# Kernel optimization log

Hardware: AMD Instinct MI355X
Metric: run time of the kernel (lower is better)

Reference implementation:

```python
import jax, jax.numpy as jnp
import numpy as np

N, E, IN_DIM, HID = 50000, 800000, 512, 256
EPS = 1e-5


def _gat_layer(x, W, a_src, a_dst, b, src, dst, n, heads, ch):
    # x: [N, F_in] -> h: [N, H, C]
    h = (x @ W).reshape(n, heads, ch)
    alpha_src = jnp.sum(h * a_src, axis=-1)  # [N, H]
    alpha_dst = jnp.sum(h * a_dst, axis=-1)  # [N, H]
    e = jax.nn.leaky_relu(alpha_src[src] + alpha_dst[dst], negative_slope=0.2)  # [E', H]
    # segment softmax over incoming edges of each destination node
    m = jax.ops.segment_max(e, dst, num_segments=n)  # [N, H]
    ex = jnp.exp(e - m[dst])
    den = jax.ops.segment_sum(ex, dst, num_segments=n)  # [N, H]
    alpha = ex / den[dst]
    out = jax.ops.segment_sum(alpha[:, :, None] * h[src], dst, num_segments=n)  # [N, H, C]
    return out.reshape(n, heads * ch) + b


def _layer_norm(x, w, b):
    mu = jnp.mean(x, axis=-1, keepdims=True)
    var = jnp.mean(jnp.square(x - mu), axis=-1, keepdims=True)
    return (x - mu) * jax.lax.rsqrt(var + EPS) * w + b


def setup_inputs() -> dict:
    key = jax.random.key(0)
    ks = jax.random.split(key, 16)
    d = {}
    d['x'] = jax.random.normal(ks[0], (N, IN_DIM), dtype=jnp.float32)
    d['edge_index'] = jax.random.randint(ks[1], (2, E), 0, N, dtype=jnp.int32)
    s = 0.05
    # layer 0: GATConv(512, 64, heads=4)
    d['W0'] = jax.random.normal(ks[2], (IN_DIM, HID), dtype=jnp.float32) * s
    d['as0'] = jax.random.normal(ks[3], (4, 64), dtype=jnp.float32) * s
    d['ad0'] = jax.random.normal(ks[4], (4, 64), dtype=jnp.float32) * s
    d['b0'] = jnp.zeros((HID,), dtype=jnp.float32)
    d['lnw0'] = jnp.ones((HID,), dtype=jnp.float32)
    d['lnb0'] = jnp.zeros((HID,), dtype=jnp.float32)
    # layer 1: GATConv(256, 64, heads=4)
    d['W1'] = jax.random.normal(ks[5], (HID, HID), dtype=jnp.float32) * s
    d['as1'] = jax.random.normal(ks[6], (4, 64), dtype=jnp.float32) * s
    d['ad1'] = jax.random.normal(ks[7], (4, 64), dtype=jnp.float32) * s
    d['b1'] = jnp.zeros((HID,), dtype=jnp.float32)
    d['lnw1'] = jnp.ones((HID,), dtype=jnp.float32)
    d['lnb1'] = jnp.zeros((HID,), dtype=jnp.float32)
    # layer 2: GATConv(256, 256, heads=1)
    d['W2'] = jax.random.normal(ks[8], (HID, HID), dtype=jnp.float32) * s
    d['as2'] = jax.random.normal(ks[9], (1, HID), dtype=jnp.float32) * s
    d['ad2'] = jax.random.normal(ks[10], (1, HID), dtype=jnp.float32) * s
    d['b2'] = jnp.zeros((HID,), dtype=jnp.float32)
    d['lnw2'] = jnp.ones((HID,), dtype=jnp.float32)
    d['lnb2'] = jnp.zeros((HID,), dtype=jnp.float32)
    return d


def reference(x, edge_index, W0, as0, ad0, b0, lnw0, lnb0,
              W1, as1, ad1, b1, lnw1, lnb1,
              W2, as2, ad2, b2, lnw2, lnb2):
    n = x.shape[0]
    loop = jnp.arange(n, dtype=edge_index.dtype)
    src = jnp.concatenate([edge_index[0], loop])  # PyG add_self_loops=True
    dst = jnp.concatenate([edge_index[1], loop])
    h = _gat_layer(x, W0, as0, ad0, b0, src, dst, n, 4, 64)
    h = jax.nn.elu(_layer_norm(h, lnw0, lnb0))
    h = _gat_layer(h, W1, as1, ad1, b1, src, dst, n, 4, 64)
    h = jax.nn.elu(_layer_norm(h, lnw1, lnb1))
    h = _gat_layer(h, W2, as2, ad2, b2, src, dst, n, 1, HID)
    h = jax.nn.elu(_layer_norm(h, lnw2, lnb2))
    return h
```

## Files before the change

kernel.cpp:

```cpp
#include <hip/hip_runtime.h>

#define HID 256
#define EPSV 1e-5f
#define ASTR 136
#define BSTR 72

typedef __bf16 bf16x8 __attribute__((ext_vector_type(8)));
typedef float  floatx4 __attribute__((ext_vector_type(4)));

static __device__ __forceinline__ ushort f2bf(float f) {
  union { float f; unsigned int i; } c; c.f = f;
  unsigned int u = c.i;
  u += 0x7FFFu + ((u >> 16) & 1u);
  return (ushort)(u >> 16);
}
static __device__ __forceinline__ float bf2f(ushort u) {
  union { unsigned int i; float f; } c; c.i = ((unsigned int)u) << 16; return c.f;
}

__global__ void count_kernel(const int* __restrict__ ei, int* __restrict__ deg, int E, int tot) {
  int i = blockIdx.x * blockDim.x + threadIdx.x;
  if (i < tot) {
    int dst = (i < E) ? ei[E + i] : (i - E);
    atomicAdd(&deg[dst], 1);
  }
}

__global__ void scanA_kernel(const int* __restrict__ deg, int* __restrict__ incl,
                             int* __restrict__ sums, int n) {
  __shared__ int buf[1024];
  const int t = threadIdx.x;
  const int i = blockIdx.x * 1024 + t;
  int x = (i < n) ? deg[i] : 0;
  buf[t] = x;
  __syncthreads();
  for (int off = 1; off < 1024; off <<= 1) {
    int v = (t >= off) ? buf[t - off] : 0;
    __syncthreads();
    buf[t] += v;
    __syncthreads();
  }
  if (i < n) incl[i] = buf[t];
  if (t == 1023) sums[blockIdx.x] = buf[1023];
}

__global__ void scanB_kernel(int* __restrict__ sums, int* __restrict__ offs, int nblk) {
  __shared__ int buf[256];
  const int t = threadIdx.x;
  int x = (t < nblk) ? sums[t] : 0;
  buf[t] = x;
  __syncthreads();
  for (int off = 1; off < 256; off <<= 1) {
    int v = (t >= off) ? buf[t - off] : 0;
    __syncthreads();
    buf[t] += v;
    __syncthreads();
  }
  if (t < nblk) offs[t] = buf[t] - x;
  if (t == nblk) offs[nblk] = buf[nblk - 1];
}

__global__ void scanC_kernel(const int* __restrict__ deg, const int* __restrict__ incl,
                             const int* __restrict__ offs, int* __restrict__ rp,
                             int* __restrict__ cur, int n, int nblk) {
  const int i = blockIdx.x * 1024 + threadIdx.x;
  if (i < n) {
    int v = offs[blockIdx.x] + incl[i] - deg[i];
    rp[i] = v;
    cur[i] = v;
  }
  if (i == 0) rp[n] = offs[nblk];
}

__global__ void scatter_kernel(const int* __restrict__ ei, int* __restrict__ cur,
                               int* __restrict__ csr, int E, int tot) {
  int i = blockIdx.x * blockDim.x + threadIdx.x;
  if (i < tot) {
    int src = (i < E) ? ei[i] : (i - E);
    int dst = (i < E) ? ei[E + i] : (i - E);
    int pos = atomicAdd(&cur[dst], 1);
    csr[pos] = src;
  }
}

__global__ __launch_bounds__(256) void transpose_kernel(
    const float* __restrict__ W, ushort* __restrict__ Wt, int K) {
  __shared__ ushort tile[32][33];
  const int tx = threadIdx.x & 31, ty = threadIdx.x >> 5;
  const int bm = blockIdx.x * 32;
  const int bk = blockIdx.y * 32;
  #pragma unroll
  for (int yy = ty; yy < 32; yy += 8)
    tile[tx][yy] = f2bf(W[(size_t)(bk + yy) * 256 + bm + tx]);
  __syncthreads();
  #pragma unroll
  for (int yy = ty; yy < 32; yy += 8)
    Wt[(size_t)(bm + yy) * K + bk + tx] = tile[yy][tx];
}

static __device__ __forceinline__ void alpha_epilogue(
    const floatx4 (&acc)[4][4], const float* __restrict__ avs,
    const float* __restrict__ avd, float* __restrict__ asrc,
    float* __restrict__ adst, int row0, int col0, int wm, int wn,
    int quad, int m16, int nrows) {
  float sv[4], dv[4];
  #pragma unroll
  for (int j = 0; j < 4; j++) {
    int col = col0 + wn + j * 16 + m16;
    sv[j] = avs[col];
    dv[j] = avd[col];
  }
  const int idx = (col0 + wn) >> 6;
  #pragma unroll
  for (int i = 0; i < 4; i++) {
    #pragma unroll
    for (int r = 0; r < 4; r++) {
      int row = row0 + wm + i * 16 + quad * 4 + r;
      float s = 0.f, d = 0.f;
      #pragma unroll
      for (int j = 0; j < 4; j++) {
        s = fmaf(acc[i][j][r], sv[j], s);
        d = fmaf(acc[i][j][r], dv[j], d);
      }
      #pragma unroll
      for (int o = 1; o < 16; o <<= 1) { s += __shfl_xor(s, o); d += __shfl_xor(d, o); }
      if (m16 == 0 && row < nrows) {
        asrc[row * 4 + idx] = s;
        adst[row * 4 + idx] = d;
      }
    }
  }
}

__global__ __launch_bounds__(256) void gemm_kernel(
    const float* __restrict__ A, const ushort* __restrict__ Bt,
    ushort* __restrict__ hb, const float* __restrict__ avs,
    const float* __restrict__ avd, float* __restrict__ asrc,
    float* __restrict__ adst, int nrows, int K) {
  __shared__ ushort At[128 * ASTR];
  __shared__ ushort Bs[128 * BSTR];
  const int tid  = threadIdx.x;
  const int lane = tid & 63;
  const int wave = tid >> 6;
  const int quad = lane >> 4;
  const int m16  = lane & 15;
  const int row0 = blockIdx.x * 128;
  const int col0 = blockIdx.y * 128;
  const int wm = (wave >> 1) * 64;
  const int wn = (wave & 1) * 64;

  floatx4 acc[4][4];
  #pragma unroll
  for (int i = 0; i < 4; i++)
    #pragma unroll
    for (int j = 0; j < 4; j++) acc[i][j] = (floatx4){0.f, 0.f, 0.f, 0.f};

  const int arow = tid >> 3;
  const int acol = (tid & 7) * 4;
  const int brow = tid >> 2;
  const int bcol = (tid & 3) * 8;

  for (int k0 = 0; k0 < K; k0 += 64) {
    floatx4 va[4][2];
    int4 vb[2][2];
    #pragma unroll
    for (int i = 0; i < 4; i++) {
      int ar = min(row0 + arow + 32 * i, nrows - 1);
      #pragma unroll
      for (int c = 0; c < 2; c++)
        va[i][c] = *(const floatx4*)(A + (size_t)ar * K + k0 + c * 32 + acol);
    }
    #pragma unroll
    for (int i = 0; i < 2; i++) {
      int r = brow + 64 * i;
      #pragma unroll
      for (int c = 0; c < 2; c++)
        vb[i][c] = *(const int4*)(Bt + (size_t)(col0 + r) * K + k0 + c * 32 + bcol);
    }
    #pragma unroll
    for (int i = 0; i < 4; i++) {
      int r = arow + 32 * i;
      #pragma unroll
      for (int c = 0; c < 2; c++) {
        floatx4 v = va[i][c];
        unsigned u0 = __float_as_uint(v[0]), u1 = __float_as_uint(v[1]);
        unsigned u2 = __float_as_uint(v[2]), u3 = __float_as_uint(v[3]);
        unsigned ph0 = __builtin_amdgcn_perm(u1, u0, 0x07060302u);
        unsigned ph1 = __builtin_amdgcn_perm(u3, u2, 0x07060302u);
        float l0 = v[0] - __uint_as_float(u0 & 0xffff0000u);
        float l1 = v[1] - __uint_as_float(u1 & 0xffff0000u);
        float l2 = v[2] - __uint_as_float(u2 & 0xffff0000u);
        float l3 = v[3] - __uint_as_float(u3 & 0xffff0000u);
        unsigned pl0 = __builtin_amdgcn_perm(__float_as_uint(l1), __float_as_uint(l0), 0x07060302u);
        unsigned pl1 = __builtin_amdgcn_perm(__float_as_uint(l3), __float_as_uint(l2), 0x07060302u);
        *(uint2*)&At[r * ASTR + c * 32 + acol]      = make_uint2(ph0, ph1);
        *(uint2*)&At[r * ASTR + 64 + c * 32 + acol] = make_uint2(pl0, pl1);
      }
    }
    #pragma unroll
    for (int i = 0; i < 2; i++) {
      int r = brow + 64 * i;
      #pragma unroll
      for (int c = 0; c < 2; c++)
        *(int4*)&Bs[r * BSTR + c * 32 + bcol] = vb[i][c];
    }
    __syncthreads();
    #pragma unroll
    for (int kk = 0; kk < 2; kk++) {
      bf16x8 bfr[4];
      #pragma unroll
      for (int j = 0; j < 4; j++)
        bfr[j] = *(const bf16x8*)&Bs[(wn + j * 16 + m16) * BSTR + kk * 32 + quad * 8];
      #pragma unroll
      for (int p = 0; p < 2; p++) {
        bf16x8 af[4];
        #pragma unroll
        for (int i = 0; i < 4; i++)
          af[i] = *(const bf16x8*)&At[(wm + i * 16 + m16) * ASTR + p * 64 + kk * 32 + quad * 8];
        #pragma unroll
        for (int i = 0; i < 4; i++)
          #pragma unroll
          for (int j = 0; j < 4; j++)
            acc[i][j] = __builtin_amdgcn_mfma_f32_16x16x32_bf16(af[i], bfr[j], acc[i][j], 0, 0, 0);
      }
    }
    __syncthreads();
  }
  #pragma unroll
  for (int i = 0; i < 4; i++) {
    int rbase = row0 + wm + i * 16 + quad * 4;
    #pragma unroll
    for (int j = 0; j < 4; j++) {
      int col = col0 + wn + j * 16 + m16;
      #pragma unroll
      for (int r = 0; r < 4; r++) {
        int row = rbase + r;
        if (row < nrows) hb[(size_t)row * HID + col] = f2bf(acc[i][j][r]);
      }
    }
  }
  alpha_epilogue(acc, avs, avd, asrc, adst, row0, col0, wm, wn, quad, m16, nrows);
}

__global__ __launch_bounds__(256) void gemm_packed_kernel(
    const ushort* __restrict__ A, const ushort* __restrict__ Bt,
    ushort* __restrict__ hb, const float* __restrict__ avs,
    const float* __restrict__ avd, float* __restrict__ asrc,
    float* __restrict__ adst, int nrows) {
  __shared__ ushort At[128 * BSTR];
  __shared__ ushort Bs[128 * BSTR];
  const int tid  = threadIdx.x;
  const int lane = tid & 63;
  const int wave = tid >> 6;
  const int quad = lane >> 4;
  const int m16  = lane & 15;
  const int row0 = blockIdx.x * 128;
  const int col0 = blockIdx.y * 128;
  const int wm = (wave >> 1) * 64;
  const int wn = (wave & 1) * 64;

  floatx4 acc[4][4];
  #pragma unroll
  for (int i = 0; i < 4; i++)
    #pragma unroll
    for (int j = 0; j < 4; j++) acc[i][j] = (floatx4){0.f, 0.f, 0.f, 0.f};

  const int srow = tid >> 2;
  const int scol = (tid & 3) * 8;

  for (int k0 = 0; k0 < 512; k0 += 64) {
    const int kb = k0 & 255;
    int4 va[2][2], vb[2][2];
    #pragma unroll
    for (int i = 0; i < 2; i++) {
      int r = srow + 64 * i;
      int ar = min(row0 + r, nrows - 1);
      #pragma unroll
      for (int c = 0; c < 2; c++) {
        va[i][c] = *(const int4*)(A + (size_t)ar * 512 + k0 + c * 32 + scol);
        vb[i][c] = *(const int4*)(Bt + (size_t)(col0 + r) * 256 + kb + c * 32 + scol);
      }
    }
    #pragma unroll
    for (int i = 0; i < 2; i++) {
      int r = srow + 64 * i;
      #pragma unroll
      for (int c = 0; c < 2; c++) {
        *(int4*)&At[r * BSTR + c * 32 + scol] = va[i][c];
        *(int4*)&Bs[r * BSTR + c * 32 + scol] = vb[i][c];
      }
    }
    __syncthreads();
    #pragma unroll
    for (int kk = 0; kk < 2; kk++) {
      bf16x8 af[4], bfr[4];
      #pragma unroll
      for (int j = 0; j < 4; j++)
        bfr[j] = *(const bf16x8*)&Bs[(wn + j * 16 + m16) * BSTR + kk * 32 + quad * 8];
      #pragma unroll
      for (int i = 0; i < 4; i++)
        af[i] = *(const bf16x8*)&At[(wm + i * 16 + m16) * BSTR + kk * 32 + quad * 8];
      #pragma unroll
      for (int i = 0; i < 4; i++)
        #pragma unroll
        for (int j = 0; j < 4; j++)
          acc[i][j] = __builtin_amdgcn_mfma_f32_16x16x32_bf16(af[i], bfr[j], acc[i][j], 0, 0, 0);
    }
    __syncthreads();
  }
  #pragma unroll
  for (int i = 0; i < 4; i++) {
    int rbase = row0 + wm + i * 16 + quad * 4;
    #pragma unroll
    for (int j = 0; j < 4; j++) {
      int col = col0 + wn + j * 16 + m16;
      #pragma unroll
      for (int r = 0; r < 4; r++) {
        int row = rbase + r;
        if (row < nrows) hb[(size_t)row * HID + col] = f2bf(acc[i][j][r]);
      }
    }
  }
  alpha_epilogue(acc, avs, avd, asrc, adst, row0, col0, wm, wn, quad, m16, nrows);
}

__global__ __launch_bounds__(256) void agg_ln_kernel(
    const ushort* __restrict__ hb, const float* __restrict__ asrc,
    const float* __restrict__ adst, const int* __restrict__ rp,
    const int* __restrict__ csr,
    const float* __restrict__ bias, const float* __restrict__ lnw,
    const float* __restrict__ lnb, ushort* __restrict__ apk,
    float* __restrict__ fout, int H, int n) {
  __shared__ float2 exs[4][64];
  const int t = threadIdx.x;
  const int w = t >> 6, lane = t & 63;
  const int nid = blockIdx.x * 4 + w;
  if (nid >= n) return;
  const int CH = (H == 4) ? 16 : 64;
  const int jj = lane & (CH - 1);
  const int hh = (H == 4) ? (lane >> 4) : 0;
  const int ch = 4 * lane;
  float ad;
  if (H == 4) {
    ad = adst[nid * 4 + hh];
  } else {
    floatx4 t4 = *(const floatx4*)(adst + nid * 4);
    ad = t4[0] + t4[1] + t4[2] + t4[3];
  }
  const int beg = rp[nid], end = rp[nid + 1];
  const char* hbase = (const char*)hb + ch * 2;
  float den = 0.f;
  float a0 = 0.f, a1 = 0.f, a2 = 0.f, a3 = 0.f;
  float b0 = 0.f, b1 = 0.f, b2 = 0.f, b3 = 0.f;
  float c0_ = 0.f, c1 = 0.f, c2 = 0.f, c3 = 0.f;
  float d0_ = 0.f, d1 = 0.f, d2 = 0.f, d3 = 0.f;

  int snext = 0;
  {
    int cnt0 = min(CH, end - beg);
    if (lane < cnt0) snext = csr[beg + lane];
  }

  for (int c0 = beg; c0 < end; c0 += CH) {
    const int cnt = min(CH, end - c0);
    int s = snext;
    const int nc0 = c0 + CH;
    if (nc0 < end) {
      int ncnt = min(CH, end - nc0);
      if (lane < ncnt) snext = csr[nc0 + lane];
    }
    s = __shfl(s, jj);
    float ex = 0.f;
    if (jj < cnt) {
      float e;
      if (H == 4) {
        e = asrc[s * 4 + hh] + ad;
      } else {
        floatx4 t4 = *(const floatx4*)(asrc + s * 4);
        e = t4[0] + t4[1] + t4[2] + t4[3] + ad;
      }
      e = (e > 0.f) ? e : 0.2f * e;
      ex = __expf(fminf(e, 60.f));
    }
    exs[w][lane] = make_float2(ex, __int_as_float(s << 9));
    float dsum = ex;
    #pragma unroll
    for (int o = 32; o > 0; o >>= 1)
      if (o < CH) dsum += __shfl_xor(dsum, o);
    den += dsum;
    const float2* exw = &exs[w][hh * CH];
    int j = 0;
    for (; j + 4 <= cnt; j += 4) {
      float2 q0 = exw[j];
      float2 q1 = exw[j + 1];
      float2 q2 = exw[j + 2];
      float2 q3 = exw[j + 3];
      uint2 u0 = *(const uint2*)(hbase + __float_as_int(q0.y));
      uint2 u1 = *(const uint2*)(hbase + __float_as_int(q1.y));
      uint2 u2 = *(const uint2*)(hbase + __float_as_int(q2.y));
      uint2 u3 = *(const uint2*)(hbase + __float_as_int(q3.y));
      a0 = fmaf(q0.x, __uint_as_float(u0.x << 16), a0);
      a1 = fmaf(q0.x, __uint_as_float(u0.x & 0xffff0000u), a1);
      a2 = fmaf(q0.x, __uint_as_float(u0.y << 16), a2);
      a3 = fmaf(q0.x, __uint_as_float(u0.y & 0xffff0000u), a3);
      b0 = fmaf(q1.x, __uint_as_float(u1.x << 16), b0);
      b1 = fmaf(q1.x, __uint_as_float(u1.x & 0xffff0000u), b1);
      b2 = fmaf(q1.x, __uint_as_float(u1.y << 16), b2);
      b3 = fmaf(q1.x, __uint_as_float(u1.y & 0xffff0000u), b3);
      c0_ = fmaf(q2.x, __uint_as_float(u2.x << 16), c0_);
      c1 = fmaf(q2.x, __uint_as_float(u2.x & 0xffff0000u), c1);
      c2 = fmaf(q2.x, __uint_as_float(u2.y << 16), c2);
      c3 = fmaf(q2.x, __uint_as_float(u2.y & 0xffff0000u), c3);
      d0_ = fmaf(q3.x, __uint_as_float(u3.x << 16), d0_);
      d1 = fmaf(q3.x, __uint_as_float(u3.x & 0xffff0000u), d1);
      d2 = fmaf(q3.x, __uint_as_float(u3.y << 16), d2);
      d3 = fmaf(q3.x, __uint_as_float(u3.y & 0xffff0000u), d3);
    }
    for (; j < cnt; ++j) {
      float2 q0 = exw[j];
      uint2 u0 = *(const uint2*)(hbase + __float_as_int(q0.y));
      a0 = fmaf(q0.x, __uint_as_float(u0.x << 16), a0);
      a1 = fmaf(q0.x, __uint_as_float(u0.x & 0xffff0000u), a1);
      a2 = fmaf(q0.x, __uint_as_float(u0.y << 16), a2);
      a3 = fmaf(q0.x, __uint_as_float(u0.y & 0xffff0000u), a3);
    }
  }
  a0 += b0 + c0_ + d0_;
  a1 += b1 + c1 + d1;
  a2 += b2 + c2 + d2;
  a3 += b3 + c3 + d3;

  const float inv = 1.f / den;
  const floatx4 bia = *(const floatx4*)(bias + ch);
  float v0 = a0 * inv + bia[0];
  float v1 = a1 * inv + bia[1];
  float v2 = a2 * inv + bia[2];
  float v3 = a3 * inv + bia[3];
  float r1 = v0 + v1 + v2 + v3;
  #pragma unroll
  for (int o = 32; o > 0; o >>= 1) r1 += __shfl_xor(r1, o);
  float mu = r1 * (1.f / HID);
  float e0 = v0 - mu, e1 = v1 - mu, e2 = v2 - mu, e3 = v3 - mu;
  float r2 = e0 * e0 + e1 * e1 + e2 * e2 + e3 * e3;
  #pragma unroll
  for (int o = 32; o > 0; o >>= 1) r2 += __shfl_xor(r2, o);
  float rstd = rsqrtf(r2 * (1.f / HID) + EPSV);
  const floatx4 wv = *(const floatx4*)(lnw + ch);
  const floatx4 bv = *(const floatx4*)(lnb + ch);
  float y0 = e0 * rstd * wv[0] + bv[0];
  float y1 = e1 * rstd * wv[1] + bv[1];
  float y2 = e2 * rstd * wv[2] + bv[2];
  float y3 = e3 * rstd * wv[3] + bv[3];
  float o0 = (y0 > 0.f) ? y0 : expm1f(y0);
  float o1 = (y1 > 0.f) ? y1 : expm1f(y1);
  float o2 = (y2 > 0.f) ? y2 : expm1f(y2);
  float o3 = (y3 > 0.f) ? y3 : expm1f(y3);
  if (apk) {
    union { ushort us[4]; unsigned long long u64; } ph, pl;
    ushort h0 = f2bf(o0), h1 = f2bf(o1), h2 = f2bf(o2), h3 = f2bf(o3);
    ph.us[0] = h0; ph.us[1] = h1; ph.us[2] = h2; ph.us[3] = h3;
    pl.us[0] = f2bf(o0 - bf2f(h0)); pl.us[1] = f2bf(o1 - bf2f(h1));
    pl.us[2] = f2bf(o2 - bf2f(h2)); pl.us[3] = f2bf(o3 - bf2f(h3));
    *(unsigned long long*)(apk + (size_t)nid * 512 + ch)       = ph.u64;
    *(unsigned long long*)(apk + (size_t)nid * 512 + 256 + ch) = pl.u64;
  } else {
    floatx4 ov; ov[0] = o0; ov[1] = o1; ov[2] = o2; ov[3] = o3;
    *(floatx4*)(fout + (size_t)nid * HID + ch) = ov;
  }
}

extern "C" void kernel_launch(void* const* d_in, const int* in_sizes, int n_in,
                              void* d_out, int out_size, void* d_ws, size_t ws_size,
                              hipStream_t stream) {
  const float* x  = (const float*)d_in[0];
  const int*   ei = (const int*)d_in[1];
  const float* Wm[3]  = {(const float*)d_in[2], (const float*)d_in[8],  (const float*)d_in[14]};
  const float* Avs[3] = {(const float*)d_in[3], (const float*)d_in[9],  (const float*)d_in[15]};
  const float* Avd[3] = {(const float*)d_in[4], (const float*)d_in[10], (const float*)d_in[16]};
  const float* Bia[3] = {(const float*)d_in[5], (const float*)d_in[11], (const float*)d_in[17]};
  const float* Lnw[3] = {(const float*)d_in[6], (const float*)d_in[12], (const float*)d_in[18]};
  const float* Lnb[3] = {(const float*)d_in[7], (const float*)d_in[13], (const float*)d_in[19]};
  const int n = in_sizes[0] / 512;
  const int E = in_sizes[1] / 2;
  const int tot = E + n;
  const int nblk = (n + 1023) / 1024;

  char* p = (char*)d_ws;
  ushort* hb   = (ushort*)p; p += (size_t)n * HID * 2;
  ushort* apk  = (ushort*)p; p += (size_t)n * 512 * 2;
  ushort* Wt   = (ushort*)p; p += 256 * 512 * 2;
  float*  asrc = (float*)p;  p += (size_t)n * 4 * 4;
  float*  adst = (float*)p;  p += (size_t)n * 4 * 4;
  int* rp   = (int*)p; p += (size_t)(n + 1) * 4;
  int* cur  = (int*)p; p += (size_t)n * 4;
  int* csr  = (int*)p; p += (size_t)tot * 4;
  int* deg  = (int*)p; p += (size_t)n * 4;
  int* incl = (int*)p; p += (size_t)n * 4;
  int* sums = (int*)p; p += (size_t)(nblk + 1) * 4;
  int* offs = (int*)p; p += (size_t)(nblk + 1) * 4;

  hipMemsetAsync(deg, 0, (size_t)n * 4, stream);
  count_kernel<<<(tot + 255) / 256, 256, 0, stream>>>(ei, deg, E, tot);
  scanA_kernel<<<nblk, 1024, 0, stream>>>(deg, incl, sums, n);
  scanB_kernel<<<1, 256, 0, stream>>>(sums, offs, nblk);
  scanC_kernel<<<nblk, 1024, 0, stream>>>(deg, incl, offs, rp, cur, n, nblk);
  scatter_kernel<<<(tot + 255) / 256, 256, 0, stream>>>(ei, cur, csr, E, tot);

  const int KB[3] = {512, 256, 256};
  const int HH[3] = {4, 4, 1};
  dim3 gg((n + 127) / 128, 2);
  for (int l = 0; l < 3; l++) {
    dim3 tg(8, KB[l] / 32);
    transpose_kernel<<<tg, 256, 0, stream>>>(Wm[l], Wt, KB[l]);
    if (l == 0)
      gemm_kernel<<<gg, 256, 0, stream>>>(x, Wt, hb, Avs[l], Avd[l], asrc, adst, n, 512);
    else
      gemm_packed_kernel<<<gg, 256, 0, stream>>>(apk, Wt, hb, Avs[l], Avd[l], asrc, adst, n);
    agg_ln_kernel<<<(n + 3) / 4, 256, 0, stream>>>(
        hb, asrc, adst, rp, csr, Bia[l], Lnw[l], Lnb[l],
        (l < 2) ? apk : (ushort*)nullptr,
        (l == 2) ? (float*)d_out : (float*)nullptr, HH[l], n);
  }
}
```

Before: 617.3 us.

## Halve GEMM row tile to 64 and simplify aggregation edge loop

Both GEMM kernels now use 64-row tiles instead of 128, so each wave holds a 2x4 accumulator array and the grid gets twice as many row blocks. The global-to-shared load mapping is also reworked so each thread reads contiguous 16-element chunks. In the aggregation kernel, the prefetch of the next chunk of CSR indices is removed and the gather loop is unrolled by 2 instead of 4. The aim is more parallelism and lower register pressure, which should raise occupancy; the cost is less B-tile reuse per block and fewer gathers in flight in the aggregation.

```diff
diff --git a/kernel.cpp b/kernel.cpp
--- a/kernel.cpp
+++ b/kernel.cpp
@@ -99,7 +99,7 @@
 }
 
 static __device__ __forceinline__ void alpha_epilogue(
-    const floatx4 (&acc)[4][4], const float* __restrict__ avs,
+    const floatx4 (&acc)[2][4], const float* __restrict__ avs,
     const float* __restrict__ avd, float* __restrict__ asrc,
     float* __restrict__ adst, int row0, int col0, int wm, int wn,
     int quad, int m16, int nrows) {
@@ -112,7 +112,7 @@
   }
   const int idx = (col0 + wn) >> 6;
   #pragma unroll
-  for (int i = 0; i < 4; i++) {
+  for (int i = 0; i < 2; i++) {
     #pragma unroll
     for (int r = 0; r < 4; r++) {
       int row = row0 + wm + i * 16 + quad * 4 + r;
@@ -137,34 +137,34 @@
     ushort* __restrict__ hb, const float* __restrict__ avs,
     const float* __restrict__ avd, float* __restrict__ asrc,
     float* __restrict__ adst, int nrows, int K) {
-  __shared__ ushort At[128 * ASTR];
+  __shared__ ushort At[64 * ASTR];
   __shared__ ushort Bs[128 * BSTR];
   const int tid  = threadIdx.x;
   const int lane = tid & 63;
   const int wave = tid >> 6;
   const int quad = lane >> 4;
   const int m16  = lane & 15;
-  const int row0 = blockIdx.x * 128;
+  const int row0 = blockIdx.x * 64;
   const int col0 = blockIdx.y * 128;
-  const int wm = (wave >> 1) * 64;
+  const int wm = (wave >> 1) * 32;
   const int wn = (wave & 1) * 64;
 
-  floatx4 acc[4][4];
-  #pragma unroll
-  for (int i = 0; i < 4; i++)
+  floatx4 acc[2][4];
+  #pragma unroll
+  for (int i = 0; i < 2; i++)
     #pragma unroll
     for (int j = 0; j < 4; j++) acc[i][j] = (floatx4){0.f, 0.f, 0.f, 0.f};
 
   const int arow = tid >> 3;
   const int acol = (tid & 7) * 4;
   const int brow = tid >> 2;
-  const int bcol = (tid & 3) * 8;
+  const int bcol = (tid & 3) * 16;
 
   for (int k0 = 0; k0 < K; k0 += 64) {
-    floatx4 va[4][2];
+    floatx4 va[2][2];
     int4 vb[2][2];
     #pragma unroll
-    for (int i = 0; i < 4; i++) {
+    for (int i = 0; i < 2; i++) {
       int ar = min(row0 + arow + 32 * i, nrows - 1);
       #pragma unroll
       for (int c = 0; c < 2; c++)
@@ -175,10 +175,10 @@
       int r = brow + 64 * i;
       #pragma unroll
       for (int c = 0; c < 2; c++)
-        vb[i][c] = *(const int4*)(Bt + (size_t)(col0 + r) * K + k0 + c * 32 + bcol);
-    }
-    #pragma unroll
-    for (int i = 0; i < 4; i++) {
+        vb[i][c] = *(const int4*)(Bt + (size_t)(col0 + r) * K + k0 + bcol + 8 * c);
+    }
+    #pragma unroll
+    for (int i = 0; i < 2; i++) {
       int r = arow + 32 * i;
       #pragma unroll
       for (int c = 0; c < 2; c++) {
@@ -202,7 +202,7 @@
       int r = brow + 64 * i;
       #pragma unroll
       for (int c = 0; c < 2; c++)
-        *(int4*)&Bs[r * BSTR + c * 32 + bcol] = vb[i][c];
+        *(int4*)&Bs[r * BSTR + bcol + 8 * c] = vb[i][c];
     }
     __syncthreads();
     #pragma unroll
@@ -213,12 +213,12 @@
         bfr[j] = *(const bf16x8*)&Bs[(wn + j * 16 + m16) * BSTR + kk * 32 + quad * 8];
       #pragma unroll
       for (int p = 0; p < 2; p++) {
-        bf16x8 af[4];
+        bf16x8 af[2];
         #pragma unroll
-        for (int i = 0; i < 4; i++)
+        for (int i = 0; i < 2; i++)
           af[i] = *(const bf16x8*)&At[(wm + i * 16 + m16) * ASTR + p * 64 + kk * 32 + quad * 8];
         #pragma unroll
-        for (int i = 0; i < 4; i++)
+        for (int i = 0; i < 2; i++)
           #pragma unroll
           for (int j = 0; j < 4; j++)
             acc[i][j] = __builtin_amdgcn_mfma_f32_16x16x32_bf16(af[i], bfr[j], acc[i][j], 0, 0, 0);
@@ -227,7 +227,7 @@
     __syncthreads();
   }
   #pragma unroll
-  for (int i = 0; i < 4; i++) {
+  for (int i = 0; i < 2; i++) {
     int rbase = row0 + wm + i * 16 + quad * 4;
     #pragma unroll
     for (int j = 0; j < 4; j++) {
@@ -247,61 +247,67 @@
     ushort* __restrict__ hb, const float* __restrict__ avs,
     const float* __restrict__ avd, float* __restrict__ asrc,
     float* __restrict__ adst, int nrows) {
-  __shared__ ushort At[128 * BSTR];
+  __shared__ ushort At[64 * BSTR];
   __shared__ ushort Bs[128 * BSTR];
   const int tid  = threadIdx.x;
   const int lane = tid & 63;
   const int wave = tid >> 6;
   const int quad = lane >> 4;
   const int m16  = lane & 15;
-  const int row0 = blockIdx.x * 128;
+  const int row0 = blockIdx.x * 64;
   const int col0 = blockIdx.y * 128;
-  const int wm = (wave >> 1) * 64;
+  const int wm = (wave >> 1) * 32;
   const int wn = (wave & 1) * 64;
 
-  floatx4 acc[4][4];
-  #pragma unroll
-  for (int i = 0; i < 4; i++)
+  floatx4 acc[2][4];
+  #pragma unroll
+  for (int i = 0; i < 2; i++)
     #pragma unroll
     for (int j = 0; j < 4; j++) acc[i][j] = (floatx4){0.f, 0.f, 0.f, 0.f};
 
-  const int srow = tid >> 2;
-  const int scol = (tid & 3) * 8;
+  const int arow = tid >> 2;
+  const int acol = (tid & 3) * 16;
+  const int brow = tid >> 2;
+  const int bcol = (tid & 3) * 16;
 
   for (int k0 = 0; k0 < 512; k0 += 64) {
     const int kb = k0 & 255;
-    int4 va[2][2], vb[2][2];
+    int4 va[2], vb[2][2];
+    {
+      int ar = min(row0 + arow, nrows - 1);
+      #pragma unroll
+      for (int c = 0; c < 2; c++)
+        va[c] = *(const int4*)(A + (size_t)ar * 512 + k0 + acol + 8 * c);
+    }
     #pragma unroll
     for (int i = 0; i < 2; i++) {
-      int r = srow + 64 * i;
-      int ar = min(row0 + r, nrows - 1);
-      #pragma unroll
-      for (int c = 0; c < 2; c++) {
-        va[i][c] = *(const int4*)(A + (size_t)ar * 512 + k0 + c * 32 + scol);
-        vb[i][c] = *(const int4*)(Bt + (size_t)(col0 + r) * 256 + kb + c * 32 + scol);
-      }
-    }
+      int r = brow + 64 * i;
+      #pragma unroll
+      for (int c = 0; c < 2; c++)
+        vb[i][c] = *(const int4*)(Bt + (size_t)(col0 + r) * 256 + kb + bcol + 8 * c);
+    }
+    #pragma unroll
+    for (int c = 0; c < 2; c++)
+      *(int4*)&At[arow * BSTR + acol + 8 * c] = va[c];
     #pragma unroll
     for (int i = 0; i < 2; i++) {
-      int r = srow + 64 * i;
-      #pragma unroll
-      for (int c = 0; c < 2; c++) {
-        *(int4*)&At[r * BSTR + c * 32 + scol] = va[i][c];
-        *(int4*)&Bs[r * BSTR + c * 32 + scol] = vb[i][c];
-      }
+      int r = brow + 64 * i;
+      #pragma unroll
+      for (int c = 0; c < 2; c++)
+        *(int4*)&Bs[r * BSTR + bcol + 8 * c] = vb[i][c];
     }
     __syncthreads();
     #pragma unroll
     for (int kk = 0; kk < 2; kk++) {
-      bf16x8 af[4], bfr[4];
+      bf16x8 af[2], bfr[4];
       #pragma unroll
       for (int j = 0; j < 4; j++)
         bfr[j] = *(const bf16x8*)&Bs[(wn + j * 16 + m16) * BSTR + kk * 32 + quad * 8];
       #pragma unroll
-      for (int i = 0; i < 4; i++)
+      for (int i = 0; i < 2; i++)
         af[i] = *(const bf16x8*)&At[(wm + i * 16 + m16) * BSTR + kk * 32 + quad * 8];
       #pragma unroll
-      for (int i = 0; i < 4; i++)
+      for (int i = 0; i < 2; i++)
         #pragma unroll
         for (int j = 0; j < 4; j++)
           acc[i][j] = __builtin_amdgcn_mfma_f32_16x16x32_bf16(af[i], bfr[j], acc[i][j], 0, 0, 0);
@@ -309,7 +315,7 @@
     __syncthreads();
   }
   #pragma unroll
-  for (int i = 0; i < 4; i++) {
+  for (int i = 0; i < 2; i++) {
     int rbase = row0 + wm + i * 16 + quad * 4;
     #pragma unroll
     for (int j = 0; j < 4; j++) {
@@ -352,23 +358,10 @@
   float den = 0.f;
   float a0 = 0.f, a1 = 0.f, a2 = 0.f, a3 = 0.f;
   float b0 = 0.f, b1 = 0.f, b2 = 0.f, b3 = 0.f;
-  float c0_ = 0.f, c1 = 0.f, c2 = 0.f, c3 = 0.f;
-  float d0_ = 0.f, d1 = 0.f, d2 = 0.f, d3 = 0.f;
-
-  int snext = 0;
-  {
-    int cnt0 = min(CH, end - beg);
-    if (lane < cnt0) snext = csr[beg + lane];
-  }
 
   for (int c0 = beg; c0 < end; c0 += CH) {
     const int cnt = min(CH, end - c0);
-    int s = snext;
-    const int nc0 = c0 + CH;
-    if (nc0 < end) {
-      int ncnt = min(CH, end - nc0);
-      if (lane < ncnt) snext = csr[nc0 + lane];
-    }
+    int s = (lane < cnt) ? csr[c0 + lane] : 0;
     s = __shfl(s, jj);
     float ex = 0.f;
     if (jj < cnt) {
@@ -390,15 +383,11 @@
     den += dsum;
     const float2* exw = &exs[w][hh * CH];
     int j = 0;
-    for (; j + 4 <= cnt; j += 4) {
+    for (; j + 2 <= cnt; j += 2) {
       float2 q0 = exw[j];
       float2 q1 = exw[j + 1];
-      float2 q2 = exw[j + 2];
-      float2 q3 = exw[j + 3];
       uint2 u0 = *(const uint2*)(hbase + __float_as_int(q0.y));
       uint2 u1 = *(const uint2*)(hbase + __float_as_int(q1.y));
-      uint2 u2 = *(const uint2*)(hbase + __float_as_int(q2.y));
-      uint2 u3 = *(const uint2*)(hbase + __float_as_int(q3.y));
       a0 = fmaf(q0.x, __uint_as_float(u0.x << 16), a0);
       a1 = fmaf(q0.x, __uint_as_float(u0.x & 0xffff0000u), a1);
       a2 = fmaf(q0.x, __uint_as_float(u0.y << 16), a2);
@@ -407,16 +396,8 @@
       b1 = fmaf(q1.x, __uint_as_float(u1.x & 0xffff0000u), b1);
       b2 = fmaf(q1.x, __uint_as_float(u1.y << 16), b2);
       b3 = fmaf(q1.x, __uint_as_float(u1.y & 0xffff0000u), b3);
-      c0_ = fmaf(q2.x, __uint_as_float(u2.x << 16), c0_);
-      c1 = fmaf(q2.x, __uint_as_float(u2.x & 0xffff0000u), c1);
-      c2 = fmaf(q2.x, __uint_as_float(u2.y << 16), c2);
-      c3 = fmaf(q2.x, __uint_as_float(u2.y & 0xffff0000u), c3);
-      d0_ = fmaf(q3.x, __uint_as_float(u3.x << 16), d0_);
-      d1 = fmaf(q3.x, __uint_as_float(u3.x & 0xffff0000u), d1);
-      d2 = fmaf(q3.x, __uint_as_float(u3.y << 16), d2);
-      d3 = fmaf(q3.x, __uint_as_float(u3.y & 0xffff0000u), d3);
-    }
-    for (; j < cnt; ++j) {
+    }
+    if (j < cnt) {
       float2 q0 = exw[j];
       uint2 u0 = *(const uint2*)(hbase + __float_as_int(q0.y));
       a0 = fmaf(q0.x, __uint_as_float(u0.x << 16), a0);
@@ -425,10 +406,7 @@
       a3 = fmaf(q0.x, __uint_as_float(u0.y & 0xffff0000u), a3);
     }
   }
-  a0 += b0 + c0_ + d0_;
-  a1 += b1 + c1 + d1;
-  a2 += b2 + c2 + d2;
-  a3 += b3 + c3 + d3;
+  a0 += b0; a1 += b1; a2 += b2; a3 += b3;
 
   const float inv = 1.f / den;
   const floatx4 bia = *(const floatx4*)(bias + ch);
@@ -508,7 +486,7 @@
 
   const int KB[3] = {512, 256, 256};
   const int HH[3] = {4, 4, 1};
-  dim3 gg((n + 127) / 128, 2);
+  dim3 gg((n + 63) / 64, 2);
   for (int l = 0; l < 3; l++) {
     dim3 tg(8, KB[l] / 32);
     transpose_kernel<<<tg, 256, 0, stream>>>(Wm[l], Wt, KB[l]);
```

Result: no change. 626.1 us (+1.4%).
